# Optimization experiments

Hardware: AMD Instinct MI355X
Metric: run time of the kernel (lower is better)

## Reference

```python
import jax, jax.numpy as jnp
import numpy as np

HIDDEN = 128
NUM_HEADS = 8
F32_MIN = jnp.finfo(jnp.float32).min


def _split_heads(x, n):
    # [B, S, D] -> [B, n, S, D//n]
    b, s, d = x.shape
    return x.reshape(b, s, n, d // n).transpose(0, 2, 1, 3)


def setup_inputs() -> dict:
    key = jax.random.key(0)
    k1, k2, k3 = jax.random.split(key, 3)
    B, S = 4, 2048
    key_and_value = jax.random.normal(k1, (B, S, 2 * HIDDEN), dtype=jnp.float32)
    query = jax.random.normal(k2, (B, S, HIDDEN), dtype=jnp.float32)
    seq_len = jax.random.randint(k3, (B, 1), 1, S + 1, dtype=jnp.int32)
    return {"key_and_value": key_and_value, "query": query, "seq_len": seq_len}


def reference(key_and_value, query, seq_len):
    B, S, _ = query.shape
    d_head = HIDDEN // NUM_HEADS
    k, v = jnp.split(key_and_value, 2, axis=2)           # each [B, S, HIDDEN]
    Q = _split_heads(query, NUM_HEADS) * (d_head ** 0.5)  # NOTE: original MULTIPLIES by sqrt(d_head)
    K = _split_heads(k, NUM_HEADS)
    V = _split_heads(v, NUM_HEADS)
    # scores: [B, H, S, S]
    logits = jnp.einsum('bhqd,bhkd->bhqk', Q, K)
    # length mask over key positions: valid where pos < seq_len (one-hot+cumsum trick)
    valid = (jnp.arange(S, dtype=jnp.int32)[None, :] < seq_len).astype(jnp.float32)  # [B, S]
    logits = logits + F32_MIN * (1.0 - valid[:, None, None, :])
    weights = jax.nn.softmax(logits, axis=-1)
    out = jnp.einsum('bhqk,bhkd->bhqd', weights, V)       # [B, H, S, d_head]
    return out.transpose(0, 2, 1, 3).reshape(B, S, HIDDEN)
```

## Files before the change

kernel.cpp:

```cpp
#include <hip/hip_runtime.h>
#include <hip/hip_bf16.h>

#define HIDDEN 128
#define NHEAD  8
#define DHEAD  16
#define KBLK   64
#define TILEB  4096
#define QSCALE 5.77078016355585277626f
#define RTHR   8.0f

typedef __attribute__((ext_vector_type(8))) _Float16 f16x8;
typedef __attribute__((ext_vector_type(4))) _Float16 f16x4;
typedef __attribute__((ext_vector_type(4))) float  f32x4;
typedef __attribute__((ext_vector_type(2))) float  f32x2;
typedef __attribute__((ext_vector_type(4))) int    i32x4;

__device__ __forceinline__ int ksub(int k)  { return ((k >> 5) << 1) | ((k >> 2) & 1); }
__device__ __forceinline__ int kirow(int k) { return (((k >> 3) & 3) << 2) | (k & 3); }

__device__ __forceinline__ void cvt_store(char* Sb, int ka, i32x4 vaddr,
                                          f32x4 kvec, f32x4 vvec)
{
    f16x4 kh;
    #pragma unroll
    for (int i = 0; i < 4; ++i) kh[i] = (_Float16)kvec[i];
    *(f16x4*)(Sb + ka) = kh;
    #pragma unroll
    for (int i = 0; i < 4; ++i)
        *(_Float16*)(Sb + vaddr[i]) = (_Float16)vvec[i];
}

template<bool SPLIT>
__global__ __launch_bounds__(256, 8)
void mha_fwd(const float* __restrict__ kv,
             const float* __restrict__ q,
             const int*   __restrict__ seq_len,
             float* __restrict__ out,
             _Float16* __restrict__ pbuf,
             float* __restrict__ mlbuf,
             int S, int nc, int chunk)
{
    const int qtile = blockIdx.x;
    const int h     = blockIdx.y;
    int b, c0;
    if (SPLIT) { const int Bn = gridDim.z / nc; b = blockIdx.z % Bn; c0 = blockIdx.z / Bn; }
    else       { b = blockIdx.z; c0 = 0; }
    const int L = seq_len[b];
    const int kstart = SPLIT ? c0 * chunk : 0;
    if (SPLIT && kstart >= L) return;
    const int kend = SPLIT ? min(L, kstart + chunk) : L;

    const int tid  = threadIdx.x;
    const int lane = tid & 63;
    const int wave = tid >> 6;
    const int g    = lane >> 4;
    const int lr   = lane & 15;
    const int sw   = (lr & 7) << 4;

    __shared__ __align__(16) char Stg[2][TILEB];

    const int qrowb = qtile * KBLK + wave * 16 + lr;
    f16x8 qf;
    {
        const float* qp = q + ((size_t)(b * S + qrowb) * HIDDEN) + h * DHEAD + (g & 1) * 8;
        #pragma unroll
        for (int j = 0; j < 8; ++j) {
            float qv = qp[j] * QSCALE;
            _Float16 hi = (_Float16)qv;
            qf[j] = (g < 2) ? hi : (_Float16)(qv - (float)hi);
        }
    }

    const int sk = tid >> 2;
    const int qd = tid & 3;
    const float* kvp = kv + ((size_t)(b * S + sk) * (2 * HIDDEN)) + h * DHEAD + 4 * qd;
    const int ka = ksub(sk) * 512 + (qd >> 1) * 256 + kirow(sk) * 16 + (qd & 1) * 8;
    i32x4 vaddr;
    #pragma unroll
    for (int i = 0; i < 4; ++i) {
        const int d = 4 * qd + i;
        vaddr[i] = 2048 + d * 128 + (((sk >> 3) * 16) ^ ((d & 7) << 4)) + (sk & 7) * 2;
    }

    f32x4 acc = {0.f, 0.f, 0.f, 0.f};
    float m = -1e30f, lsum = 0.f;

    const int ntiles = (kend - kstart + KBLK - 1) >> 6;

    {
        const float* kp = kvp + (size_t)kstart * (2 * HIDDEN);
        f32x4 kvec = *(const f32x4*)kp;
        f32x4 vvec = *(const f32x4*)(kp + HIDDEN);
        cvt_store(&Stg[0][0], ka, vaddr, kvec, vvec);
    }
    __syncthreads();

    for (int ti = 0; ti < ntiles; ++ti) {
        const int kb = kstart + ti * KBLK;
        const char* Sb = &Stg[ti & 1][0];
        const bool hasnext = (ti + 1) < ntiles;

        f32x4 nkv, nvv;
        if (hasnext) {
            const float* kp = kvp + (size_t)(kb + KBLK) * (2 * HIDDEN);
            nkv = *(const f32x4*)kp;
            nvv = *(const f32x4*)(kp + HIDDEN);
        }

        f16x8 kf[4];
        #pragma unroll
        for (int sub = 0; sub < 4; ++sub)
            kf[sub] = *(const f16x8*)(Sb + sub * 512 + (g & 1) * 256 + lr * 16);
        f16x8 vb0 = *(const f16x8*)(Sb + 2048 + lr * 128 + ((g * 16) ^ sw));
        f16x8 vb1 = *(const f16x8*)(Sb + 2048 + lr * 128 + ((64 + g * 16) ^ sw));

        f32x4 s[4];
        #pragma unroll
        for (int sub = 0; sub < 4; ++sub) {
            f32x4 z = {0.f, 0.f, 0.f, 0.f};
            s[sub] = __builtin_amdgcn_mfma_f32_16x16x32_f16(kf[sub], qf, z, 0, 0, 0);
        }
        if (kb + KBLK > kend) {
            #pragma unroll
            for (int sub = 0; sub < 4; ++sub) {
                const int kb2 = kb + (sub >> 1) * 32 + (sub & 1) * 4 + g * 8;
                #pragma unroll
                for (int r = 0; r < 4; ++r)
                    if (kb2 + r >= kend) s[sub][r] = -1e30f;
            }
        }

        float t0 = fmaxf(fmaxf(s[0][0], s[0][1]), fmaxf(s[0][2], s[0][3]));
        float t1 = fmaxf(fmaxf(s[1][0], s[1][1]), fmaxf(s[1][2], s[1][3]));
        float t2 = fmaxf(fmaxf(s[2][0], s[2][1]), fmaxf(s[2][2], s[2][3]));
        float t3 = fmaxf(fmaxf(s[3][0], s[3][1]), fmaxf(s[3][2], s[3][3]));
        float pmax = fmaxf(fmaxf(t0, t1), fmaxf(t2, t3));

        if (__any(pmax > m + RTHR)) {
            float tmax = fmaxf(pmax, __shfl_xor(pmax, 16));
            tmax = fmaxf(tmax, __shfl_xor(tmax, 32));
            const float mn = fmaxf(m, tmax);
            const float alpha = exp2f(m - mn);
            m = mn;
            lsum *= alpha;
            acc *= alpha;
        }
        const float mn = m;

        float rsum = 0.f;
        f16x8 pa0, pa1;
        #pragma unroll
        for (int sub = 0; sub < 2; ++sub)
            #pragma unroll
            for (int r = 0; r < 4; ++r) {
                float p = exp2f(s[sub][r] - mn);
                rsum += p;
                pa0[sub * 4 + r] = (_Float16)p;
            }
        #pragma unroll
        for (int sub = 2; sub < 4; ++sub)
            #pragma unroll
            for (int r = 0; r < 4; ++r) {
                float p = exp2f(s[sub][r] - mn);
                rsum += p;
                pa1[(sub - 2) * 4 + r] = (_Float16)p;
            }
        lsum += rsum;

        acc = __builtin_amdgcn_mfma_f32_16x16x32_f16(vb0, pa0, acc, 0, 0, 0);
        acc = __builtin_amdgcn_mfma_f32_16x16x32_f16(vb1, pa1, acc, 0, 0, 0);

        if (hasnext)
            cvt_store(&Stg[(ti + 1) & 1][0], ka, vaddr, nkv, nvv);
        __syncthreads();
    }

    lsum += __shfl_xor(lsum, 16);
    lsum += __shfl_xor(lsum, 32);
    if (SPLIT) {
        const size_t row = (((size_t)b * nc + c0) * S + qrowb) * NHEAD + h;
        f16x4 pk;
        #pragma unroll
        for (int r = 0; r < 4; ++r) pk[r] = (_Float16)acc[r];
        *(f16x4*)&pbuf[row * DHEAD + g * 4] = pk;
        if (g == 0) { f32x2 ml = {m, lsum}; *(f32x2*)&mlbuf[row * 2] = ml; }
    } else {
        const float inv = 1.0f / lsum;
        *(f32x4*)&out[((size_t)b * S + qrowb) * HIDDEN + h * DHEAD + g * 4] = acc * inv;
    }
}

__global__ __launch_bounds__(256)
void mha_merge(const _Float16* __restrict__ pbuf, const float* __restrict__ mlbuf,
               const int* __restrict__ seq_len, float* __restrict__ out,
               int S, int nc, int chunk)
{
    const int t = blockIdx.x * 256 + threadIdx.x;
    const int h = t & (NHEAD - 1);
    const int rest = t >> 3;
    const int qg = rest % S;
    const int b  = rest / S;
    const int L  = seq_len[b];
    const int nch = min(nc, (L + chunk - 1) / chunk);

    const size_t cstr = (size_t)S * NHEAD;
    const size_t row0 = ((size_t)b * nc) * cstr + (size_t)qg * NHEAD + h;

    float mv[8], lv[8];
    float M = -1e30f;
    for (int c = 0; c < nch; ++c) {
        f32x2 ml = *(const f32x2*)&mlbuf[(row0 + c * cstr) * 2];
        mv[c] = ml[0]; lv[c] = ml[1];
        M = fmaxf(M, ml[0]);
    }
    float den = 0.f;
    float o[16];
    #pragma unroll
    for (int i = 0; i < 16; ++i) o[i] = 0.f;
    for (int c = 0; c < nch; ++c) {
        float w = exp2f(mv[c] - M);
        den += w * lv[c];
        const _Float16* pp = &pbuf[(row0 + c * cstr) * DHEAD];
        f16x8 p0 = *(const f16x8*)&pp[0];
        f16x8 p1 = *(const f16x8*)&pp[8];
        #pragma unroll
        for (int i = 0; i < 8; ++i) {
            o[i]     += w * (float)p0[i];
            o[i + 8] += w * (float)p1[i];
        }
    }
    const float inv = 1.0f / den;
    float* op = &out[((size_t)b * S + qg) * HIDDEN + h * DHEAD];
    #pragma unroll
    for (int i = 0; i < 4; ++i) {
        f32x4 v = {o[4*i] * inv, o[4*i+1] * inv, o[4*i+2] * inv, o[4*i+3] * inv};
        *(f32x4*)&op[4 * i] = v;
    }
}

extern "C" void kernel_launch(void* const* d_in, const int* in_sizes, int n_in,
                              void* d_out, int out_size, void* d_ws, size_t ws_size,
                              hipStream_t stream)
{
    const float* kv      = (const float*)d_in[0];
    const float* query   = (const float*)d_in[1];
    const int*   seq_len = (const int*)d_in[2];
    float* out           = (float*)d_out;

    const int B = in_sizes[2];
    const int S = in_sizes[1] / (B * HIDDEN);

    const int chunk = 512;
    const int nc = (S + chunk - 1) / chunk;
    const size_t mlb = (size_t)B * nc * S * NHEAD * 2 * sizeof(float);
    const size_t pbb = (size_t)B * nc * S * NHEAD * DHEAD * sizeof(_Float16);

    if (nc <= 8 && ws_size >= mlb + pbb) {
        float* mlbuf = (float*)d_ws;
        _Float16* pbuf = (_Float16*)((char*)d_ws + mlb);
        mha_fwd<true><<<dim3(S / KBLK, NHEAD, B * nc), dim3(256), 0, stream>>>(
            kv, query, seq_len, nullptr, pbuf, mlbuf, S, nc, chunk);
        const int nrows = B * S * NHEAD;
        mha_merge<<<dim3((nrows + 255) / 256), dim3(256), 0, stream>>>(
            pbuf, mlbuf, seq_len, out, S, nc, chunk);
    } else {
        mha_fwd<false><<<dim3(S / KBLK, NHEAD, B), dim3(256), 0, stream>>>(
            kv, query, seq_len, out, nullptr, nullptr, S, 1, S);
    }
}
```

Measured before the change: 41.66 us.

## Use single-wave blocks with direct K loads and transposed LDS reads for V

New measurement: 101.9 us. 2.45x slower.

```diff
diff --git a/kernel.cpp b/kernel.cpp
--- a/kernel.cpp
+++ b/kernel.cpp
@@ -5,33 +5,29 @@
 #define NHEAD  8
 #define DHEAD  16
 #define KBLK   64
-#define TILEB  4096
+#define QBLK   16
 #define QSCALE 5.77078016355585277626f
 #define RTHR   8.0f
 
 typedef __attribute__((ext_vector_type(8))) _Float16 f16x8;
 typedef __attribute__((ext_vector_type(4))) _Float16 f16x4;
+typedef __attribute__((ext_vector_type(8))) float  f32x8;
 typedef __attribute__((ext_vector_type(4))) float  f32x4;
 typedef __attribute__((ext_vector_type(2))) float  f32x2;
-typedef __attribute__((ext_vector_type(4))) int    i32x4;
-
-__device__ __forceinline__ int ksub(int k)  { return ((k >> 5) << 1) | ((k >> 2) & 1); }
-__device__ __forceinline__ int kirow(int k) { return (((k >> 3) & 3) << 2) | (k & 3); }
-
-__device__ __forceinline__ void cvt_store(char* Sb, int ka, i32x4 vaddr,
-                                          f32x4 kvec, f32x4 vvec)
-{
-    f16x4 kh;
-    #pragma unroll
-    for (int i = 0; i < 4; ++i) kh[i] = (_Float16)kvec[i];
-    *(f16x4*)(Sb + ka) = kh;
-    #pragma unroll
-    for (int i = 0; i < 4; ++i)
-        *(_Float16*)(Sb + vaddr[i]) = (_Float16)vvec[i];
+
+#define TR_READ(dst, addr, imm) \
+    asm volatile("ds_read_b64_tr_b16 %0, %1 offset:" imm : "=v"(dst) : "v"(addr) : "memory")
+
+__device__ __forceinline__ int permrow(int k) {
+    return (k & 3) | (((k >> 3) & 3) << 2) | (((k >> 2) & 1) << 4) | ((k >> 5) << 5);
+}
+
+__device__ __forceinline__ int keyof(int sub, int lr) {
+    return 32 * (sub >> 1) + (lr >> 2) * 8 + (sub & 1) * 4 + (lr & 3);
 }
 
 template<bool SPLIT>
-__global__ __launch_bounds__(256, 8)
+__global__ __launch_bounds__(64, 4)
 void mha_fwd(const float* __restrict__ kv,
              const float* __restrict__ q,
              const int*   __restrict__ seq_len,
@@ -50,19 +46,16 @@
     if (SPLIT && kstart >= L) return;
     const int kend = SPLIT ? min(L, kstart + chunk) : L;
 
-    const int tid  = threadIdx.x;
-    const int lane = tid & 63;
-    const int wave = tid >> 6;
+    const int lane = threadIdx.x;
     const int g    = lane >> 4;
     const int lr   = lane & 15;
-    const int sw   = (lr & 7) << 4;
-
-    __shared__ __align__(16) char Stg[2][TILEB];
-
-    const int qrowb = qtile * KBLK + wave * 16 + lr;
+
+    __shared__ __align__(16) _Float16 Vst[2][64][16];
+
+    const int qrow = qtile * QBLK + lr;
     f16x8 qf;
     {
-        const float* qp = q + ((size_t)(b * S + qrowb) * HIDDEN) + h * DHEAD + (g & 1) * 8;
+        const float* qp = q + ((size_t)(b * S + qrow) * HIDDEN) + h * DHEAD + (g & 1) * 8;
         #pragma unroll
         for (int j = 0; j < 8; ++j) {
             float qv = qp[j] * QSCALE;
@@ -71,48 +64,61 @@
         }
     }
 
-    const int sk = tid >> 2;
-    const int qd = tid & 3;
-    const float* kvp = kv + ((size_t)(b * S + sk) * (2 * HIDDEN)) + h * DHEAD + 4 * qd;
-    const int ka = ksub(sk) * 512 + (qd >> 1) * 256 + kirow(sk) * 16 + (qd & 1) * 8;
-    i32x4 vaddr;
+    const float* kp[4];
     #pragma unroll
-    for (int i = 0; i < 4; ++i) {
-        const int d = 4 * qd + i;
-        vaddr[i] = 2048 + d * 128 + (((sk >> 3) * 16) ^ ((d & 7) << 4)) + (sk & 7) * 2;
-    }
+    for (int sub = 0; sub < 4; ++sub)
+        kp[sub] = kv + ((size_t)(b * S + kstart + keyof(sub, lr)) * (2 * HIDDEN))
+                     + h * DHEAD + (g & 1) * 8;
+    const float* vp = kv + ((size_t)(b * S + kstart + lane) * (2 * HIDDEN)) + HIDDEN + h * DHEAD;
+    const int KSTRIDE = KBLK * 2 * HIDDEN;
+
+    const unsigned vbase0 = (unsigned)(unsigned long long)(const void*)&Vst[0][0][0] + lane * 8;
+    const int pr = permrow(lane);
 
     f32x4 acc = {0.f, 0.f, 0.f, 0.f};
     float m = -1e30f, lsum = 0.f;
 
     const int ntiles = (kend - kstart + KBLK - 1) >> 6;
 
+    f16x8 kf[4];
     {
-        const float* kp = kvp + (size_t)kstart * (2 * HIDDEN);
-        f32x4 kvec = *(const f32x4*)kp;
-        f32x4 vvec = *(const f32x4*)(kp + HIDDEN);
-        cvt_store(&Stg[0][0], ka, vaddr, kvec, vvec);
-    }
-    __syncthreads();
-
+        f32x8 kn[4];
+        f32x4 vn[4];
+        #pragma unroll
+        for (int sub = 0; sub < 4; ++sub) kn[sub] = *(const f32x8*)kp[sub];
+        #pragma unroll
+        for (int i = 0; i < 4; ++i) vn[i] = *(const f32x4*)(vp + 4 * i);
+        #pragma unroll
+        for (int sub = 0; sub < 4; ++sub)
+            #pragma unroll
+            for (int j = 0; j < 8; ++j) kf[sub][j] = (_Float16)kn[sub][j];
+        f16x8 w0, w1;
+        #pragma unroll
+        for (int i = 0; i < 4; ++i) {
+            w0[i] = (_Float16)vn[0][i]; w0[i + 4] = (_Float16)vn[1][i];
+            w1[i] = (_Float16)vn[2][i]; w1[i + 4] = (_Float16)vn[3][i];
+        }
+        *(f16x8*)&Vst[0][pr][0] = w0;
+        *(f16x8*)&Vst[0][pr][8] = w1;
+    }
+
+    int cur = 0;
     for (int ti = 0; ti < ntiles; ++ti) {
         const int kb = kstart + ti * KBLK;
-        const char* Sb = &Stg[ti & 1][0];
         const bool hasnext = (ti + 1) < ntiles;
 
-        f32x4 nkv, nvv;
+        f32x8 kn[4];
+        f32x4 vn[4];
         if (hasnext) {
-            const float* kp = kvp + (size_t)(kb + KBLK) * (2 * HIDDEN);
-            nkv = *(const f32x4*)kp;
-            nvv = *(const f32x4*)(kp + HIDDEN);
-        }
-
-        f16x8 kf[4];
-        #pragma unroll
-        for (int sub = 0; sub < 4; ++sub)
-            kf[sub] = *(const f16x8*)(Sb + sub * 512 + (g & 1) * 256 + lr * 16);
-        f16x8 vb0 = *(const f16x8*)(Sb + 2048 + lr * 128 + ((g * 16) ^ sw));
-        f16x8 vb1 = *(const f16x8*)(Sb + 2048 + lr * 128 + ((64 + g * 16) ^ sw));
+            #pragma unroll
+            for (int sub = 0; sub < 4; ++sub) {
+                kp[sub] += KSTRIDE;
+                kn[sub] = *(const f32x8*)kp[sub];
+            }
+            vp += KSTRIDE;
+            #pragma unroll
+            for (int i = 0; i < 4; ++i) vn[i] = *(const f32x4*)(vp + 4 * i);
+        }
 
         f32x4 s[4];
         #pragma unroll
@@ -135,13 +141,12 @@
         float t2 = fmaxf(fmaxf(s[2][0], s[2][1]), fmaxf(s[2][2], s[2][3]));
         float t3 = fmaxf(fmaxf(s[3][0], s[3][1]), fmaxf(s[3][2], s[3][3]));
         float pmax = fmaxf(fmaxf(t0, t1), fmaxf(t2, t3));
-
         if (__any(pmax > m + RTHR)) {
             float tmax = fmaxf(pmax, __shfl_xor(pmax, 16));
             tmax = fmaxf(tmax, __shfl_xor(tmax, 32));
-            const float mn = fmaxf(m, tmax);
-            const float alpha = exp2f(m - mn);
-            m = mn;
+            const float mn2 = fmaxf(m, tmax);
+            const float alpha = exp2f(m - mn2);
+            m = mn2;
             lsum *= alpha;
             acc *= alpha;
         }
@@ -167,18 +172,44 @@
             }
         lsum += rsum;
 
+        f16x4 v0, v1, v2, v3;
+        const unsigned va = vbase0 + (unsigned)(cur * 2048);
+        TR_READ(v0, va, "0");
+        TR_READ(v1, va, "512");
+        TR_READ(v2, va, "1024");
+        TR_READ(v3, va, "1536");
+        asm volatile("s_waitcnt lgkmcnt(0)" ::: "memory");
+        __builtin_amdgcn_sched_barrier(0);
+        f16x8 vb0, vb1;
+        #pragma unroll
+        for (int i = 0; i < 4; ++i) {
+            vb0[i] = v0[i]; vb0[i + 4] = v1[i];
+            vb1[i] = v2[i]; vb1[i + 4] = v3[i];
+        }
         acc = __builtin_amdgcn_mfma_f32_16x16x32_f16(vb0, pa0, acc, 0, 0, 0);
         acc = __builtin_amdgcn_mfma_f32_16x16x32_f16(vb1, pa1, acc, 0, 0, 0);
 
-        if (hasnext)
-            cvt_store(&Stg[(ti + 1) & 1][0], ka, vaddr, nkv, nvv);
-        __syncthreads();
+        if (hasnext) {
+            #pragma unroll
+            for (int sub = 0; sub < 4; ++sub)
+                #pragma unroll
+                for (int j = 0; j < 8; ++j) kf[sub][j] = (_Float16)kn[sub][j];
+            f16x8 w0, w1;
+            #pragma unroll
+            for (int i = 0; i < 4; ++i) {
+                w0[i] = (_Float16)vn[0][i]; w0[i + 4] = (_Float16)vn[1][i];
+                w1[i] = (_Float16)vn[2][i]; w1[i + 4] = (_Float16)vn[3][i];
+            }
+            *(f16x8*)&Vst[cur ^ 1][pr][0] = w0;
+            *(f16x8*)&Vst[cur ^ 1][pr][8] = w1;
+            cur ^= 1;
+        }
     }
 
     lsum += __shfl_xor(lsum, 16);
     lsum += __shfl_xor(lsum, 32);
     if (SPLIT) {
-        const size_t row = (((size_t)b * nc + c0) * S + qrowb) * NHEAD + h;
+        const size_t row = (((size_t)b * nc + c0) * S + qrow) * NHEAD + h;
         f16x4 pk;
         #pragma unroll
         for (int r = 0; r < 4; ++r) pk[r] = (_Float16)acc[r];
@@ -186,7 +217,7 @@
         if (g == 0) { f32x2 ml = {m, lsum}; *(f32x2*)&mlbuf[row * 2] = ml; }
     } else {
         const float inv = 1.0f / lsum;
-        *(f32x4*)&out[((size_t)b * S + qrowb) * HIDDEN + h * DHEAD + g * 4] = acc * inv;
+        *(f32x4*)&out[((size_t)b * S + qrow) * HIDDEN + h * DHEAD + g * 4] = acc * inv;
     }
 }
 
@@ -258,13 +289,13 @@
     if (nc <= 8 && ws_size >= mlb + pbb) {
         float* mlbuf = (float*)d_ws;
         _Float16* pbuf = (_Float16*)((char*)d_ws + mlb);
-        mha_fwd<true><<<dim3(S / KBLK, NHEAD, B * nc), dim3(256), 0, stream>>>(
+        mha_fwd<true><<<dim3(S / QBLK, NHEAD, B * nc), dim3(64), 0, stream>>>(
             kv, query, seq_len, nullptr, pbuf, mlbuf, S, nc, chunk);
         const int nrows = B * S * NHEAD;
         mha_merge<<<dim3((nrows + 255) / 256), dim3(256), 0, stream>>>(
             pbuf, mlbuf, seq_len, out, S, nc, chunk);
     } else {
-        mha_fwd<false><<<dim3(S / KBLK, NHEAD, B), dim3(256), 0, stream>>>(
+        mha_fwd<false><<<dim3(S / QBLK, NHEAD, B), dim3(64), 0, stream>>>(
             kv, query, seq_len, out, nullptr, nullptr, S, 1, S);
     }
 }
```
